# Kernel tuning notes

Measured on AMD Instinct MI355X. Metric: run time of the kernel, lower is better.

## Reference

```python
import jax, jax.numpy as jnp
import numpy as np

B, C, H, W = 8, 512, 32, 32
N_HEADS = 4
D_K = C // N_HEADS  # 128


def setup_inputs() -> dict:
    key = jax.random.key(0)
    k1, k2, k3, k4, k5 = jax.random.split(key, 5)
    x = jax.random.normal(k1, (B, C, H, W), dtype=jnp.float32)
    # projection: Linear(in_ch, n_heads*d_k*3)
    Wp = jax.random.normal(k2, (C, N_HEADS * D_K * 3), dtype=jnp.float32) * (C ** -0.5)
    bp = jax.random.normal(k3, (N_HEADS * D_K * 3,), dtype=jnp.float32) * 0.01
    # output: Linear(n_heads*d_k, in_ch)
    Wo = jax.random.normal(k4, (N_HEADS * D_K, C), dtype=jnp.float32) * ((N_HEADS * D_K) ** -0.5)
    bo = jax.random.normal(k5, (C,), dtype=jnp.float32) * 0.01
    return {"x": x, "Wp": Wp, "bp": bp, "Wo": Wo, "bo": bo}


def reference(x, Wp, bp, Wo, bo):
    b, c, h, w = x.shape
    scale = D_K ** -0.5
    # [B, C, H, W] -> [B, N, C], N = H*W
    xs = x.reshape(b, c, h * w).transpose(0, 2, 1)
    qkv = (xs @ Wp + bp).reshape(b, h * w, N_HEADS, 3 * D_K)
    q, k, v = jnp.split(qkv, 3, axis=-1)  # each [B, N, H, D]
    attn = jnp.einsum('bihd,bjhd->bijh', q, k) * scale
    attn = jax.nn.softmax(attn, axis=2)  # softmax over j (keys)
    out = jnp.einsum('bijh,bjhd->bihd', attn, v)
    out = out.reshape(b, h * w, N_HEADS * D_K)
    out = out @ Wo + bo
    out = out + xs  # residual (note: GroupNorm is unused in the original forward)
    return out.transpose(0, 2, 1).reshape(b, c, h, w)
```

## Files before the change

### kernel.cpp

```cpp
#include <hip/hip_runtime.h>

#define NB 8
#define NC 512
#define NTOK 1024
#define NHEADS 4
#define DKH 128

typedef unsigned short u16;
typedef __attribute__((ext_vector_type(8))) short bf16x8;
typedef __attribute__((ext_vector_type(4))) float f32x4;

__device__ inline u16 f2b(float f) {
    union { float f; unsigned u; } v; v.f = f;
    unsigned r = v.u + 0x7fffu + ((v.u >> 16) & 1u);
    return (u16)(r >> 16);
}

__device__ __forceinline__ void gll16(const u16* g, u16* l) {
    __builtin_amdgcn_global_load_lds((const __attribute__((address_space(1))) unsigned*)g,
                                     (__attribute__((address_space(3))) unsigned*)l, 16, 0, 0);
}

__global__ __launch_bounds__(256) void prep(const float* __restrict__ x, const float* __restrict__ Wp,
                                            const float* __restrict__ Wo,
                                            u16* __restrict__ xsb, u16* __restrict__ WpT, u16* __restrict__ WoT)
{
    __shared__ float tile[32][33];
    const int z = blockIdx.z;
    const float* src; u16* dst; int R, Cc;
    if (z == 0)      { src = Wp; dst = WpT; R = 512; Cc = 1536; }
    else if (z == 1) { if (blockIdx.x >= 16) return; src = Wo; dst = WoT; R = 512; Cc = 512; }
    else             { if (blockIdx.x >= 32) return;
                       src = x + (long)(z-2)*NC*NTOK; dst = xsb + (long)(z-2)*NTOK*NC; R = NC; Cc = NTOK; }
    int c0 = blockIdx.x * 32, r0 = blockIdx.y * 32;
    int tx = threadIdx.x, ty = threadIdx.y;
    #pragma unroll
    for (int k = 0; k < 4; ++k)
        tile[ty + 8*k][tx] = src[(long)(r0 + ty + 8*k) * Cc + c0 + tx];
    __syncthreads();
    #pragma unroll
    for (int k = 0; k < 4; ++k)
        dst[(long)(c0 + ty + 8*k) * R + r0 + tx] = f2b(tile[tx][ty + 8*k]);
}

__global__ __launch_bounds__(256) void gemm_qkv(const u16* __restrict__ WpT, const u16* __restrict__ xsb,
                                                const float* __restrict__ bp,
                                                u16* __restrict__ qg, u16* __restrict__ kg, u16* __restrict__ vg)
{
    __shared__ union SmU {
        struct { u16 As[128][64]; u16 Bs[128][64]; } s;
        u16 Os[4][64][72];
    } sm;
    const int tid = threadIdx.x;
    const int m0 = blockIdx.x * 128;
    const int n0 = blockIdx.y * 128;
    const int w = tid >> 6, lane = tid & 63, quad = lane >> 4, lc = lane & 15;
    const int mo = (w & 1) * 64, no = (w >> 1) * 64;
    const int sw8 = (((lane & 7) ^ (lane >> 3)) << 3);
    const int xs = lc & 7;

    f32x4 acc[4][4] = {};

    for (int k0 = 0; k0 < NC; k0 += 64) {
        __syncthreads();
        #pragma unroll
        for (int p = 0; p < 4; ++p) {
            int row = w*32 + p*8 + (lane >> 3);
            gll16(&WpT[(long)(m0 + row) * NC + k0 + sw8], &sm.s.As[w*32 + p*8][0]);
            gll16(&xsb[(long)(n0 + row) * NC + k0 + sw8], &sm.s.Bs[w*32 + p*8][0]);
        }
        __syncthreads();
        #pragma unroll
        for (int ks = 0; ks < 2; ++ks) {
            bf16x8 af[4], bfr[4];
            #pragma unroll
            for (int t = 0; t < 4; ++t) {
                af[t]  = *(const bf16x8*)&sm.s.As[mo + t*16 + lc][((ks*4 + quad) ^ xs) << 3];
                bfr[t] = *(const bf16x8*)&sm.s.Bs[no + t*16 + lc][((ks*4 + quad) ^ xs) << 3];
            }
            #pragma unroll
            for (int mt = 0; mt < 4; ++mt)
                #pragma unroll
                for (int nt = 0; nt < 4; ++nt)
                    acc[mt][nt] = __builtin_amdgcn_mfma_f32_16x16x32_bf16(af[mt], bfr[nt], acc[mt][nt], 0, 0, 0);
        }
    }
    __syncthreads();

    const int bb = n0 >> 10;
    const int nblk = n0 & 1023;
    const int cqb = m0 + mo;
    const int h = cqb / 384;
    const int rem = cqb - h * 384;
    const int sel = rem >> 7;
    const int d_base = rem & 127;

    #pragma unroll
    for (int mt = 0; mt < 4; ++mt) {
        int cq0 = cqb + mt*16 + quad*4;
        float b0 = bp[cq0+0], b1 = bp[cq0+1], b2 = bp[cq0+2], b3 = bp[cq0+3];
        #pragma unroll
        for (int nt = 0; nt < 4; ++nt) {
            f32x4 a = acc[mt][nt];
            int nl = nt*16 + lc;
            int ml = mt*16 + quad*4;
            u16 e0 = f2b(a[0]+b0), e1 = f2b(a[1]+b1), e2 = f2b(a[2]+b2), e3 = f2b(a[3]+b3);
            if (sel == 2) {
                sm.Os[w][ml+0][nl] = e0; sm.Os[w][ml+1][nl] = e1;
                sm.Os[w][ml+2][nl] = e2; sm.Os[w][ml+3][nl] = e3;
            } else {
                sm.Os[w][nl][ml+0] = e0; sm.Os[w][nl][ml+1] = e1;
                sm.Os[w][nl][ml+2] = e2; sm.Os[w][nl][ml+3] = e3;
            }
        }
    }
    __builtin_amdgcn_sched_barrier(0);

    const long bhbase = (long)(bb * NHEADS + h);
    const int sw = sw8;
    if (sel == 2) {
        #pragma unroll
        for (int pass = 0; pass < 8; ++pass) {
            int ml  = pass*8 + (lane >> 3);
            int nl0 = (lane & 7) * 8;
            bf16x8 vv = *(const bf16x8*)&sm.Os[w][ml][nl0];
            *(bf16x8*)&vg[((bhbase*DKH + d_base + ml) << 10) + nblk + no + sw] = vv;
        }
    } else if (sel == 1) {
        #pragma unroll
        for (int pass = 0; pass < 8; ++pass) {
            int nl  = pass*8 + (lane >> 3);
            int ml0 = (lane & 7) * 8;
            bf16x8 vv = *(const bf16x8*)&sm.Os[w][nl][ml0];
            *(bf16x8*)&kg[((bhbase*NTOK + nblk + no + nl) << 7) + d_base + sw] = vv;
        }
    } else {
        #pragma unroll
        for (int pass = 0; pass < 8; ++pass) {
            int nl  = pass*8 + (lane >> 3);
            int ml0 = (lane & 7) * 8;
            bf16x8 vv = *(const bf16x8*)&sm.Os[w][nl][ml0];
            *(bf16x8*)&qg[((bhbase*NTOK + nblk + no + nl) << 7) + d_base + ml0] = vv;
        }
    }
}

__global__ __launch_bounds__(512) void attn(const u16* __restrict__ qg, const u16* __restrict__ kg,
                                            const u16* __restrict__ vtg, u16* __restrict__ ho)
{
    __shared__ u16 Ks[2][64*128];
    __shared__ u16 Vt[2][128*64];
    __shared__ u16 Ps[8][16][72];
    const int tid = threadIdx.x;
    const int w = tid >> 6, lane = tid & 63, quad = lane >> 4, lc = lane & 15;
    const int id = blockIdx.x;
    const int xcd = id & 7, rest = id >> 3, sub = rest & 3, bx = rest >> 2;
    const int pr = xcd + sub*8;
    const int b = pr >> 2, h = pr & 3;
    const int i0 = bx*128 + w*16;
    const long bh = (long)(b * NHEADS + h) << 17;
    const u16* qb = qg + bh;
    const u16* kb = kg + bh;
    const u16* vb = vtg + bh;
    const float SL2E = 0.08838834764831845f * 1.4426950408889634f;

    bf16x8 qf[4];
    #pragma unroll
    for (int ks = 0; ks < 4; ++ks)
        qf[ks] = *(const bf16x8*)&qb[(long)(i0 + lc) * DKH + ks*32 + quad*8];

    f32x4 o[8] = {};
    float lsum = 0.f;
    const int xs = lc & 7;

    #pragma unroll
    for (int p = 0; p < 2; ++p) {
        int ck = (w*2 + p)*64 + lane;
        gll16(&kb[(long)ck * 8], &Ks[0][(w*2 + p)*512]);
        gll16(&vb[(((long)(ck >> 3)) << 10) + (ck & 7)*8], &Vt[0][(w*2 + p)*512]);
    }

    for (int t = 0; t < 16; ++t) {
        __syncthreads();
        if (t < 15) {
            long jo = (long)(t+1) * 64;
            #pragma unroll
            for (int p = 0; p < 2; ++p) {
                int ck = (w*2 + p)*64 + lane;
                gll16(&kb[jo*128 + (long)ck*8], &Ks[(t+1)&1][(w*2 + p)*512]);
                gll16(&vb[(((long)(ck >> 3)) << 10) + jo + (ck & 7)*8], &Vt[(t+1)&1][(w*2 + p)*512]);
            }
        }
        const u16* K = Ks[t&1];
        const u16* V = Vt[t&1];

        f32x4 s[4] = {};
        #pragma unroll
        for (int ks = 0; ks < 4; ++ks)
            #pragma unroll
            for (int jt = 0; jt < 4; ++jt) {
                bf16x8 kf = *(const bf16x8*)&K[(jt*16 + lc)*128 + (((ks*4 + quad) ^ xs) << 3)];
                s[jt] = __builtin_amdgcn_mfma_f32_16x16x32_bf16(kf, qf[ks], s[jt], 0, 0, 0);
            }

        #pragma unroll
        for (int jt = 0; jt < 4; ++jt) {
            float p0 = __builtin_amdgcn_exp2f(s[jt][0] * SL2E);
            float p1 = __builtin_amdgcn_exp2f(s[jt][1] * SL2E);
            float p2 = __builtin_amdgcn_exp2f(s[jt][2] * SL2E);
            float p3 = __builtin_amdgcn_exp2f(s[jt][3] * SL2E);
            lsum += (p0 + p1) + (p2 + p3);
            ushort4 pk;
            pk.x = f2b(p0); pk.y = f2b(p1); pk.z = f2b(p2); pk.w = f2b(p3);
            *(ushort4*)&Ps[w][lc][jt*16 + quad*4] = pk;
        }
        __builtin_amdgcn_sched_barrier(0);

        #pragma unroll
        for (int ks2 = 0; ks2 < 2; ++ks2) {
            bf16x8 pf = *(const bf16x8*)&Ps[w][lc][ks2*32 + quad*8];
            #pragma unroll
            for (int dt = 0; dt < 8; ++dt) {
                bf16x8 vf = *(const bf16x8*)&V[(dt*16 + lc)*64 + (((ks2*4 + quad) ^ xs) << 3)];
                o[dt] = __builtin_amdgcn_mfma_f32_16x16x32_bf16(vf, pf, o[dt], 0, 0, 0);
            }
        }
    }

    lsum += __shfl_xor(lsum, 16);
    lsum += __shfl_xor(lsum, 32);
    float inv = 1.0f / lsum;

    #pragma unroll
    for (int dt = 0; dt < 8; ++dt) {
        ushort4 pk;
        pk.x = f2b(o[dt][0] * inv); pk.y = f2b(o[dt][1] * inv);
        pk.z = f2b(o[dt][2] * inv); pk.w = f2b(o[dt][3] * inv);
        *(ushort4*)&ho[(long)(b*NTOK + i0 + lc) * NC + h*DKH + dt*16 + quad*4] = pk;
    }
}

__global__ __launch_bounds__(256) void gemm_out(const u16* __restrict__ WoT, const u16* __restrict__ ho,
                                                const float* __restrict__ bo, const float* __restrict__ xin,
                                                float* __restrict__ dout)
{
    __shared__ struct { u16 As[128][64]; u16 Bs[64][64]; } sm;
    const int tid = threadIdx.x;
    const int m0 = blockIdx.x * 128;
    const int n0 = blockIdx.y * 64;
    const int w = tid >> 6, lane = tid & 63, quad = lane >> 4, lc = lane & 15;
    const int mo = (w & 1) * 64, no = (w >> 1) * 32;
    const int sw8 = (((lane & 7) ^ (lane >> 3)) << 3);
    const int xs = lc & 7;

    f32x4 acc[4][2] = {};

    for (int k0 = 0; k0 < NC; k0 += 64) {
        __syncthreads();
        #pragma unroll
        for (int p = 0; p < 4; ++p) {
            int row = w*32 + p*8 + (lane >> 3);
            gll16(&WoT[(long)(m0 + row) * NC + k0 + sw8], &sm.As[w*32 + p*8][0]);
        }
        #pragma unroll
        for (int p = 0; p < 2; ++p) {
            int row = w*16 + p*8 + (lane >> 3);
            gll16(&ho[(long)(n0 + row) * NC + k0 + sw8], &sm.Bs[w*16 + p*8][0]);
        }
        __syncthreads();
        #pragma unroll
        for (int ks = 0; ks < 2; ++ks) {
            bf16x8 af[4], bfr[2];
            #pragma unroll
            for (int t = 0; t < 4; ++t)
                af[t] = *(const bf16x8*)&sm.As[mo + t*16 + lc][((ks*4 + quad) ^ xs) << 3];
            #pragma unroll
            for (int t = 0; t < 2; ++t)
                bfr[t] = *(const bf16x8*)&sm.Bs[no + t*16 + lc][((ks*4 + quad) ^ xs) << 3];
            #pragma unroll
            for (int mt = 0; mt < 4; ++mt)
                #pragma unroll
                for (int nt = 0; nt < 2; ++nt)
                    acc[mt][nt] = __builtin_amdgcn_mfma_f32_16x16x32_bf16(af[mt], bfr[nt], acc[mt][nt], 0, 0, 0);
        }
    }

    const int bb = n0 >> 10;
    #pragma unroll
    for (int mt = 0; mt < 4; ++mt) {
        int cc0 = m0 + mo + mt*16 + quad*4;
        float b0 = bo[cc0+0], b1 = bo[cc0+1], b2 = bo[cc0+2], b3 = bo[cc0+3];
        #pragma unroll
        for (int nt = 0; nt < 2; ++nt) {
            int nl = (n0 + no + nt*16 + lc) & (NTOK - 1);
            f32x4 a = acc[mt][nt];
            long ix = ((long)(bb*NC + cc0) << 10) + nl;
            dout[ix]             = a[0] + b0 + xin[ix];
            dout[ix + (1 << 10)] = a[1] + b1 + xin[ix + (1 << 10)];
            dout[ix + (2 << 10)] = a[2] + b2 + xin[ix + (2 << 10)];
            dout[ix + (3 << 10)] = a[3] + b3 + xin[ix + (3 << 10)];
        }
    }
}

extern "C" void kernel_launch(void* const* d_in, const int* in_sizes, int n_in,
                              void* d_out, int out_size, void* d_ws, size_t ws_size,
                              hipStream_t stream)
{
    (void)in_sizes; (void)n_in; (void)out_size; (void)ws_size;
    const float* x  = (const float*)d_in[0];
    const float* Wp = (const float*)d_in[1];
    const float* bp = (const float*)d_in[2];
    const float* Wo = (const float*)d_in[3];
    const float* bo = (const float*)d_in[4];
    float* out = (float*)d_out;

    u16* ws  = (u16*)d_ws;
    u16* xsb = ws;
    u16* WpT = xsb + (long)NB * NTOK * NC;
    u16* WoT = WpT + 1536L * 512;
    u16* qg  = WoT + 512L * 512;
    u16* kg  = qg + (long)NB * NHEADS * NTOK * DKH;
    u16* vtg = kg + (long)NB * NHEADS * NTOK * DKH;
    u16* ho  = vtg + (long)NB * NHEADS * NTOK * DKH;

    prep<<<dim3(48, 16, 10), dim3(32, 8), 0, stream>>>(x, Wp, Wo, xsb, WpT, WoT);
    gemm_qkv<<<dim3(1536/128, (NB*NTOK)/128), 256, 0, stream>>>(WpT, xsb, bp, qg, kg, vtg);
    attn<<<dim3(256), 512, 0, stream>>>(qg, kg, vtg, ho);
    gemm_out<<<dim3(NC/128, (NB*NTOK)/64), 256, 0, stream>>>(WoT, ho, bo, x, out);
}
```

Measured before the change: 140.7 us.

## Process two 16-row query tiles per wave in attention to reuse K/V fragments

```diff
diff --git a/kernel.cpp b/kernel.cpp
--- a/kernel.cpp
+++ b/kernel.cpp
@@ -145,39 +145,41 @@
     }
 }
 
-__global__ __launch_bounds__(512) void attn(const u16* __restrict__ qg, const u16* __restrict__ kg,
+__global__ __launch_bounds__(256) void attn(const u16* __restrict__ qg, const u16* __restrict__ kg,
                                             const u16* __restrict__ vtg, u16* __restrict__ ho)
 {
     __shared__ u16 Ks[2][64*128];
     __shared__ u16 Vt[2][128*64];
-    __shared__ u16 Ps[8][16][72];
+    __shared__ u16 Ps[4][32][72];
     const int tid = threadIdx.x;
     const int w = tid >> 6, lane = tid & 63, quad = lane >> 4, lc = lane & 15;
     const int id = blockIdx.x;
     const int xcd = id & 7, rest = id >> 3, sub = rest & 3, bx = rest >> 2;
     const int pr = xcd + sub*8;
     const int b = pr >> 2, h = pr & 3;
-    const int i0 = bx*128 + w*16;
+    const int i0 = bx*128 + w*32;
     const long bh = (long)(b * NHEADS + h) << 17;
     const u16* qb = qg + bh;
     const u16* kb = kg + bh;
     const u16* vb = vtg + bh;
     const float SL2E = 0.08838834764831845f * 1.4426950408889634f;
 
-    bf16x8 qf[4];
-    #pragma unroll
-    for (int ks = 0; ks < 4; ++ks)
-        qf[ks] = *(const bf16x8*)&qb[(long)(i0 + lc) * DKH + ks*32 + quad*8];
-
-    f32x4 o[8] = {};
-    float lsum = 0.f;
+    bf16x8 qf[2][4];
+    #pragma unroll
+    for (int ib = 0; ib < 2; ++ib)
+        #pragma unroll
+        for (int ks = 0; ks < 4; ++ks)
+            qf[ib][ks] = *(const bf16x8*)&qb[(long)(i0 + ib*16 + lc) * DKH + ks*32 + quad*8];
+
+    f32x4 o[2][8] = {};
+    float lsum[2] = {0.f, 0.f};
     const int xs = lc & 7;
 
     #pragma unroll
-    for (int p = 0; p < 2; ++p) {
-        int ck = (w*2 + p)*64 + lane;
-        gll16(&kb[(long)ck * 8], &Ks[0][(w*2 + p)*512]);
-        gll16(&vb[(((long)(ck >> 3)) << 10) + (ck & 7)*8], &Vt[0][(w*2 + p)*512]);
+    for (int p = 0; p < 4; ++p) {
+        int ck = (w*4 + p)*64 + lane;
+        gll16(&kb[(long)ck * 8], &Ks[0][(w*4 + p)*512]);
+        gll16(&vb[(((long)(ck >> 3)) << 10) + (ck & 7)*8], &Vt[0][(w*4 + p)*512]);
     }
 
     for (int t = 0; t < 16; ++t) {
@@ -185,58 +187,66 @@
         if (t < 15) {
             long jo = (long)(t+1) * 64;
             #pragma unroll
-            for (int p = 0; p < 2; ++p) {
-                int ck = (w*2 + p)*64 + lane;
-                gll16(&kb[jo*128 + (long)ck*8], &Ks[(t+1)&1][(w*2 + p)*512]);
-                gll16(&vb[(((long)(ck >> 3)) << 10) + jo + (ck & 7)*8], &Vt[(t+1)&1][(w*2 + p)*512]);
+            for (int p = 0; p < 4; ++p) {
+                int ck = (w*4 + p)*64 + lane;
+                gll16(&kb[jo*128 + (long)ck*8], &Ks[(t+1)&1][(w*4 + p)*512]);
+                gll16(&vb[(((long)(ck >> 3)) << 10) + jo + (ck & 7)*8], &Vt[(t+1)&1][(w*4 + p)*512]);
             }
         }
         const u16* K = Ks[t&1];
         const u16* V = Vt[t&1];
 
-        f32x4 s[4] = {};
+        f32x4 s[2][4] = {};
         #pragma unroll
         for (int ks = 0; ks < 4; ++ks)
             #pragma unroll
             for (int jt = 0; jt < 4; ++jt) {
                 bf16x8 kf = *(const bf16x8*)&K[(jt*16 + lc)*128 + (((ks*4 + quad) ^ xs) << 3)];
-                s[jt] = __builtin_amdgcn_mfma_f32_16x16x32_bf16(kf, qf[ks], s[jt], 0, 0, 0);
-            }
-
-        #pragma unroll
-        for (int jt = 0; jt < 4; ++jt) {
-            float p0 = __builtin_amdgcn_exp2f(s[jt][0] * SL2E);
-            float p1 = __builtin_amdgcn_exp2f(s[jt][1] * SL2E);
-            float p2 = __builtin_amdgcn_exp2f(s[jt][2] * SL2E);
-            float p3 = __builtin_amdgcn_exp2f(s[jt][3] * SL2E);
-            lsum += (p0 + p1) + (p2 + p3);
-            ushort4 pk;
-            pk.x = f2b(p0); pk.y = f2b(p1); pk.z = f2b(p2); pk.w = f2b(p3);
-            *(ushort4*)&Ps[w][lc][jt*16 + quad*4] = pk;
-        }
+                s[0][jt] = __builtin_amdgcn_mfma_f32_16x16x32_bf16(kf, qf[0][ks], s[0][jt], 0, 0, 0);
+                s[1][jt] = __builtin_amdgcn_mfma_f32_16x16x32_bf16(kf, qf[1][ks], s[1][jt], 0, 0, 0);
+            }
+
+        #pragma unroll
+        for (int ib = 0; ib < 2; ++ib)
+            #pragma unroll
+            for (int jt = 0; jt < 4; ++jt) {
+                float p0 = __builtin_amdgcn_exp2f(s[ib][jt][0] * SL2E);
+                float p1 = __builtin_amdgcn_exp2f(s[ib][jt][1] * SL2E);
+                float p2 = __builtin_amdgcn_exp2f(s[ib][jt][2] * SL2E);
+                float p3 = __builtin_amdgcn_exp2f(s[ib][jt][3] * SL2E);
+                lsum[ib] += (p0 + p1) + (p2 + p3);
+                ushort4 pk;
+                pk.x = f2b(p0); pk.y = f2b(p1); pk.z = f2b(p2); pk.w = f2b(p3);
+                *(ushort4*)&Ps[w][ib*16 + lc][jt*16 + quad*4] = pk;
+            }
         __builtin_amdgcn_sched_barrier(0);
 
         #pragma unroll
         for (int ks2 = 0; ks2 < 2; ++ks2) {
-            bf16x8 pf = *(const bf16x8*)&Ps[w][lc][ks2*32 + quad*8];
+            bf16x8 pf0 = *(const bf16x8*)&Ps[w][lc][ks2*32 + quad*8];
+            bf16x8 pf1 = *(const bf16x8*)&Ps[w][16 + lc][ks2*32 + quad*8];
             #pragma unroll
             for (int dt = 0; dt < 8; ++dt) {
                 bf16x8 vf = *(const bf16x8*)&V[(dt*16 + lc)*64 + (((ks2*4 + quad) ^ xs) << 3)];
-                o[dt] = __builtin_amdgcn_mfma_f32_16x16x32_bf16(vf, pf, o[dt], 0, 0, 0);
-            }
-        }
-    }
-
-    lsum += __shfl_xor(lsum, 16);
-    lsum += __shfl_xor(lsum, 32);
-    float inv = 1.0f / lsum;
-
-    #pragma unroll
-    for (int dt = 0; dt < 8; ++dt) {
-        ushort4 pk;
-        pk.x = f2b(o[dt][0] * inv); pk.y = f2b(o[dt][1] * inv);
-        pk.z = f2b(o[dt][2] * inv); pk.w = f2b(o[dt][3] * inv);
-        *(ushort4*)&ho[(long)(b*NTOK + i0 + lc) * NC + h*DKH + dt*16 + quad*4] = pk;
+                o[0][dt] = __builtin_amdgcn_mfma_f32_16x16x32_bf16(vf, pf0, o[0][dt], 0, 0, 0);
+                o[1][dt] = __builtin_amdgcn_mfma_f32_16x16x32_bf16(vf, pf1, o[1][dt], 0, 0, 0);
+            }
+        }
+    }
+
+    #pragma unroll
+    for (int ib = 0; ib < 2; ++ib) {
+        float l = lsum[ib];
+        l += __shfl_xor(l, 16);
+        l += __shfl_xor(l, 32);
+        float inv = 1.0f / l;
+        #pragma unroll
+        for (int dt = 0; dt < 8; ++dt) {
+            ushort4 pk;
+            pk.x = f2b(o[ib][dt][0] * inv); pk.y = f2b(o[ib][dt][1] * inv);
+            pk.z = f2b(o[ib][dt][2] * inv); pk.w = f2b(o[ib][dt][3] * inv);
+            *(ushort4*)&ho[(long)(b*NTOK + i0 + ib*16 + lc) * NC + h*DKH + dt*16 + quad*4] = pk;
+        }
     }
 }
 
@@ -326,6 +336,6 @@
 
     prep<<<dim3(48, 16, 10), dim3(32, 8), 0, stream>>>(x, Wp, Wo, xsb, WpT, WoT);
     gemm_qkv<<<dim3(1536/128, (NB*NTOK)/128), 256, 0, stream>>>(WpT, xsb, bp, qg, kg, vtg);
-    attn<<<dim3(256), 512, 0, stream>>>(qg, kg, vtg, ho);
+    attn<<<dim3(256), 256, 0, stream>>>(qg, kg, vtg, ho);
     gemm_out<<<dim3(NC/128, (NB*NTOK)/64), 256, 0, stream>>>(WoT, ho, bo, x, out);
 }
```

Measured after the change: 144.9 us. 3.0% more time.
